# Kernel optimization log

Hardware: AMD Instinct MI355X
Metric: run time of the kernel (lower is better)

## Reference

```python
import jax, jax.numpy as jnp
import numpy as np

N = 100000      # nodes
E = 1600000     # edges (avg degree 16)
F_IN = 512      # input node features
H = 8           # heads in conv1
D = 8           # per-head dim in conv1
C = 7           # classes
NEG_SLOPE = 0.2 # PyG GATConv default leaky_relu slope


def setup_inputs() -> dict:
    key = jax.random.key(0)
    ks = jax.random.split(key, 10)
    s = 0.05
    return {
        "x": jax.random.normal(ks[0], (N, F_IN), jnp.float32),
        "edge_index": jax.random.randint(ks[1], (2, E), 0, N, dtype=jnp.int64),
        "W1": jax.random.normal(ks[2], (F_IN, H * D), jnp.float32) * s,
        "a1_src": jax.random.normal(ks[3], (H, D), jnp.float32) * s,
        "a1_dst": jax.random.normal(ks[4], (H, D), jnp.float32) * s,
        "b1": jnp.zeros((H * D,), jnp.float32),
        "W2": jax.random.normal(ks[5], (H * D, C), jnp.float32) * s,
        "a2_src": jax.random.normal(ks[6], (1, C), jnp.float32) * s,
        "a2_dst": jax.random.normal(ks[7], (1, C), jnp.float32) * s,
        "b2": jnp.zeros((C,), jnp.float32),
    }


def _gat_conv(x, src, dst, W, a_src, a_dst, b, heads, dim, concat, n):
    # linear transform -> [N, H, D]
    h = (x @ W).reshape(n, heads, dim)
    # per-node attention halves: [N, H]
    al_src = jnp.einsum('nhd,hd->nh', h, a_src)
    al_dst = jnp.einsum('nhd,hd->nh', h, a_dst)
    # per-edge logits, leaky relu: [E', H]
    e = jax.nn.leaky_relu(al_src[src] + al_dst[dst], NEG_SLOPE)
    # segment softmax over incoming edges of each dst node
    m = jax.lax.stop_gradient(jax.ops.segment_max(e, dst, num_segments=n))
    p = jnp.exp(e - m[dst])
    z = jax.ops.segment_sum(p, dst, num_segments=n)
    alpha = p / z[dst]                                   # [E', H]
    # weighted scatter-add of source messages -> [N, H, D]
    out = jax.ops.segment_sum(h[src] * alpha[..., None], dst, num_segments=n)
    out = out.reshape(n, heads * dim) if concat else out.mean(axis=1)
    return out + b


def reference(x, edge_index, W1, a1_src, a1_dst, b1, W2, a2_src, a2_dst, b2):
    n = x.shape[0]
    # PyG GATConv default: add self loops
    loops = jnp.arange(n, dtype=edge_index.dtype)
    src = jnp.concatenate([edge_index[0], loops])
    dst = jnp.concatenate([edge_index[1], loops])
    h = _gat_conv(x, src, dst, W1, a1_src, a1_dst, b1, H, D, True, n)
    h = jax.nn.elu(h)
    out = _gat_conv(h, src, dst, W2, a2_src, a2_dst, b2, 1, C, False, n)
    return jax.nn.log_softmax(out, axis=1)
```

## Files before the change

kernel.cpp:

```cpp
#include <hip/hip_runtime.h>
#include <math.h>

#define N_NODES 100000
#define N_EDGES 1600000
#define F_IN 512
#define HD 64
#define CC 7
#define NKT (F_IN / 32)
#define BS 64
#define NBK ((N_NODES + BS - 1) / BS)
#define ECAP 2048
#define SCHUNK 4096
#define SBLK ((N_EDGES + SCHUNK - 1) / SCHUNK)

typedef __attribute__((ext_vector_type(8))) short short8;
typedef __attribute__((ext_vector_type(4))) float f32x4;

__device__ inline unsigned short f2bf(float f) {
    union { float f; unsigned u; } v; v.f = f;
    unsigned u = v.u;
    return (unsigned short)((u + 0x7fffu + ((u >> 16) & 1u)) >> 16);
}
__device__ inline float bf2f(unsigned short b) {
    union { unsigned u; float f; } v; v.u = ((unsigned)b) << 16;
    return v.f;
}

__global__ void zerob_kernel(int* __restrict__ bcur) {
    int i = blockIdx.x * 1024 + threadIdx.x;
    if (i < NBK) bcur[i] = 0;
}

__global__ void w1prep_kernel(const float* __restrict__ W1,
                              unsigned short* __restrict__ wf) {
    int t = blockIdx.x * 256 + threadIdx.x;
    if (t >= NKT * 4 * 64) return;
    int lane = t & 63;
    int ct = (t >> 6) & 3;
    int kt = t >> 8;
    int k0 = kt * 32 + (lane >> 4) * 8;
    int col = ct * 16 + (lane & 15);
    unsigned short* dst = wf + (size_t)t * 8;
    #pragma unroll
    for (int j = 0; j < 8; ++j) dst[j] = f2bf(W1[(k0 + j) * HD + col]);
}

__global__ __launch_bounds__(256) void gemm1att_kernel(const float* __restrict__ x,
                                                       const unsigned short* __restrict__ wf,
                                                       const float* __restrict__ a1s,
                                                       const float* __restrict__ a1d,
                                                       unsigned short* __restrict__ h1b,
                                                       float* __restrict__ als,
                                                       float* __restrict__ ald) {
    __shared__ float ls[64][65];
    const int wave = threadIdx.x >> 6;
    const int lane = threadIdx.x & 63;
    int arow = blockIdx.x * 64 + wave * 16 + (lane & 15);
    if (arow >= N_NODES) arow = N_NODES - 1;
    const float* xp = x + (size_t)arow * F_IN + (lane >> 4) * 8;
    const short8* wp = (const short8*)wf;

    f32x4 acc[4] = {};
    #pragma unroll 4
    for (int kt = 0; kt < NKT; ++kt) {
        f32x4 a0 = *(const f32x4*)(xp + kt * 32);
        f32x4 a1 = *(const f32x4*)(xp + kt * 32 + 4);
        union { short8 s; unsigned short u[8]; } af;
        af.u[0] = f2bf(a0.x); af.u[1] = f2bf(a0.y);
        af.u[2] = f2bf(a0.z); af.u[3] = f2bf(a0.w);
        af.u[4] = f2bf(a1.x); af.u[5] = f2bf(a1.y);
        af.u[6] = f2bf(a1.z); af.u[7] = f2bf(a1.w);
        #pragma unroll
        for (int ct = 0; ct < 4; ++ct) {
            short8 bf = wp[kt * 256 + ct * 64 + lane];
            acc[ct] = __builtin_amdgcn_mfma_f32_16x16x32_bf16(af.s, bf, acc[ct], 0, 0, 0);
        }
    }
    const int lrow_base = wave * 16 + (lane >> 4) * 4;
    const int ocol = lane & 15;
    #pragma unroll
    for (int ct = 0; ct < 4; ++ct) {
        #pragma unroll
        for (int r = 0; r < 4; ++r) {
            int lrow = lrow_base + r;
            int orow = blockIdx.x * 64 + lrow;
            ls[lrow][ct * 16 + ocol] = acc[ct][r];
            if (orow < N_NODES)
                h1b[(size_t)orow * HD + ct * 16 + ocol] = f2bf(acc[ct][r]);
        }
    }
    __syncthreads();
    #pragma unroll
    for (int task = threadIdx.x; task < 64 * 8; task += 256) {
        int r = task >> 3, h = task & 7;
        int node = blockIdx.x * 64 + r;
        if (node < N_NODES) {
            float s = 0.f, d = 0.f;
            #pragma unroll
            for (int k = 0; k < 8; ++k) {
                float v = ls[r][h * 8 + k];
                s += v * a1s[h * 8 + k];
                d += v * a1d[h * 8 + k];
            }
            als[node * 8 + h] = s;
            ald[node * 8 + h] = d;
        }
    }
}

__global__ __launch_bounds__(256) void binscatter_kernel(const int* __restrict__ ei,
                                                         int* __restrict__ bcur,
                                                         int2* __restrict__ pairs) {
    __shared__ int cnt[NBK];
    __shared__ int bas[NBK];
    const int e0 = blockIdx.x * SCHUNK;
    int e1 = e0 + SCHUNK; if (e1 > N_EDGES) e1 = N_EDGES;
    for (int b = threadIdx.x; b < NBK; b += 256) cnt[b] = 0;
    __syncthreads();
    for (int i = e0 + threadIdx.x; i < e1; i += 256)
        atomicAdd(&cnt[ei[N_EDGES + i] >> 6], 1);
    __syncthreads();
    for (int b = threadIdx.x; b < NBK; b += 256) {
        int c = cnt[b];
        bas[b] = c ? atomicAdd(&bcur[b], c) : 0;
        cnt[b] = 0;
    }
    __syncthreads();
    for (int i = e0 + threadIdx.x; i < e1; i += 256) {
        int s = ei[i];
        int t = ei[N_EDGES + i];
        int b = t >> 6;
        int pos = bas[b] + atomicAdd(&cnt[b], 1);
        if (pos < ECAP) pairs[(size_t)b * ECAP + pos] = make_int2(s, t);
    }
}

__global__ __launch_bounds__(256) void sortcsr_kernel(const int* __restrict__ bcur,
                                                      const int2* __restrict__ pairs,
                                                      int* __restrict__ csr_src,
                                                      int* __restrict__ rowptr,
                                                      int* __restrict__ rowcnt) {
    __shared__ int cnt[BS];
    __shared__ int start[BS];
    __shared__ int srcl[ECAP];
    const int tid = threadIdx.x;
    const int lane = tid & 63;
    const int n0 = blockIdx.x * BS;
    const size_t bbase = (size_t)blockIdx.x * ECAP;
    const int2* bp = pairs + bbase;
    int ne = bcur[blockIdx.x]; if (ne > ECAP) ne = ECAP;
    if (tid < BS) cnt[tid] = 0;
    __syncthreads();
    for (int k = tid; k < ne; k += 256)
        atomicAdd(&cnt[bp[k].y & (BS - 1)], 1);
    __syncthreads();
    if (tid < 64) {
        int a = cnt[lane];
        int xx = a;
        #pragma unroll
        for (int o = 1; o < 64; o <<= 1) { int u = __shfl_up(xx, o, 64); if (lane >= o) xx += u; }
        start[lane] = xx - a;
        cnt[lane] = 0;
    }
    __syncthreads();
    for (int k = tid; k < ne; k += 256) {
        int2 pr = bp[k];
        int ln = pr.y & (BS - 1);
        int pos = start[ln] + atomicAdd(&cnt[ln], 1);
        srcl[pos] = pr.x;
    }
    __syncthreads();
    for (int k = tid; k < ne; k += 256) csr_src[bbase + k] = srcl[k];
    if (tid < BS) {
        int node = n0 + tid;
        if (node < N_NODES) {
            rowptr[node] = (int)bbase + start[tid];
            rowcnt[node] = cnt[tid];
        }
    }
}

__global__ __launch_bounds__(256) void gather1_kernel(
        const int* __restrict__ rowptr, const int* __restrict__ rowcnt,
        const int* __restrict__ csr_src,
        const float* __restrict__ als, const float* __restrict__ ald,
        const unsigned short* __restrict__ h1b, const float* __restrict__ b1,
        const float* __restrict__ W2, const float* __restrict__ a2s,
        const float* __restrict__ a2d,
        unsigned short* __restrict__ g2b, float* __restrict__ al2s,
        float* __restrict__ al2d) {
    int node = (blockIdx.x * 256 + threadIdx.x) >> 6;
    if (node >= N_NODES) return;
    const int lane = threadIdx.x & 63;
    const int h = lane >> 3;
    const int e8 = lane & 7, base8 = lane & 56;
    const int rs = rowptr[node], ncnt = rowcnt[node];
    const float aldt = ald[node * 8 + h];
    float e = als[node * 8 + h] + aldt;
    e = (e >= 0.f) ? e : 0.2f * e;
    float p = __expf(e);
    float acc = p * bf2f(h1b[(size_t)node * HD + lane]);
    float z = p;
    int k = 0;
    for (; k + 8 <= ncnt; k += 8) {
        int s_own = csr_src[rs + k + e8];
        int se[8];
        #pragma unroll
        for (int q = 0; q < 8; ++q) se[q] = __shfl(s_own, base8 | q, 64);
        float ve[8];
        #pragma unroll
        for (int q = 0; q < 8; ++q) ve[q] = bf2f(h1b[(size_t)se[q] * HD + lane]);
        float ee = als[s_own * 8 + h] + aldt;
        ee = (ee >= 0.f) ? ee : 0.2f * ee;
        float pv = __expf(ee);
        #pragma unroll
        for (int q = 0; q < 8; ++q) {
            float pe = __shfl(pv, base8 | q, 64);
            z += pe;
            acc = fmaf(pe, ve[q], acc);
        }
    }
    if (k < ncnt) {
        const int m = ncnt - k;
        int idx = rs + k + ((e8 < m) ? e8 : (m - 1));
        int s_own = csr_src[idx];
        int se[8];
        #pragma unroll
        for (int q = 0; q < 8; ++q) se[q] = __shfl(s_own, base8 | q, 64);
        float ee = als[s_own * 8 + h] + aldt;
        ee = (ee >= 0.f) ? ee : 0.2f * ee;
        float pv = __expf(ee);
        for (int q = 0; q < m; ++q) {
            float pe = __shfl(pv, base8 | q, 64);
            float ve = bf2f(h1b[(size_t)se[q] * HD + lane]);
            z += pe;
            acc = fmaf(pe, ve, acc);
        }
    }
    float v = acc / z + b1[lane];
    v = (v > 0.f) ? v : (__expf(v) - 1.f);
    float w[CC];
    #pragma unroll
    for (int c = 0; c < CC; ++c) w[c] = W2[lane * CC + c];
    float g[CC];
    #pragma unroll
    for (int c = 0; c < CC; ++c) {
        float r = v * w[c];
        #pragma unroll
        for (int d = 1; d < 64; d <<= 1) r += __shfl_xor(r, d, 64);
        g[c] = r;
    }
    float s2 = 0.f, d2 = 0.f;
    #pragma unroll
    for (int c = 0; c < CC; ++c) { s2 += g[c] * a2s[c]; d2 += g[c] * a2d[c]; }
    if (lane < CC) g2b[(size_t)node * 8 + lane] = f2bf(g[lane]);
    if (lane == CC) g2b[(size_t)node * 8 + CC] = 0;
    if (lane == 8) al2s[node] = s2;
    if (lane == 9) al2d[node] = d2;
}

__global__ __launch_bounds__(256) void gather2_kernel(
        const int* __restrict__ rowptr, const int* __restrict__ rowcnt,
        const int* __restrict__ csr_src,
        const float* __restrict__ al2s, const float* __restrict__ al2d,
        const unsigned short* __restrict__ g2b, const float* __restrict__ b2,
        float* __restrict__ out) {
    int gid = blockIdx.x * 256 + threadIdx.x;
    int n = gid >> 3, c = gid & 7;
    if (n >= N_NODES) return;
    const int lane = threadIdx.x & 63;
    const int base8 = lane & 56;
    const int rs = rowptr[n], ncnt = rowcnt[n];
    const float adn = al2d[n];
    float e = al2s[n] + adn;
    e = (e >= 0.f) ? e : 0.2f * e;
    float p = __expf(e);
    float acc = p * bf2f(g2b[(size_t)n * 8 + c]);
    float z = p;
    int k = 0;
    for (; k + 8 <= ncnt; k += 8) {
        int s_own = csr_src[rs + k + c];
        int se[8];
        #pragma unroll
        for (int q = 0; q < 8; ++q) se[q] = __shfl(s_own, base8 | q, 64);
        float ve[8];
        #pragma unroll
        for (int q = 0; q < 8; ++q) ve[q] = bf2f(g2b[(size_t)se[q] * 8 + c]);
        float ee = al2s[s_own] + adn;
        ee = (ee >= 0.f) ? ee : 0.2f * ee;
        float pv = __expf(ee);
        #pragma unroll
        for (int q = 0; q < 8; ++q) {
            float pe = __shfl(pv, base8 | q, 64);
            z += pe;
            acc = fmaf(pe, ve[q], acc);
        }
    }
    if (k < ncnt) {
        const int m = ncnt - k;
        int idx = rs + k + ((c < m) ? c : (m - 1));
        int s_own = csr_src[idx];
        int se[8];
        #pragma unroll
        for (int q = 0; q < 8; ++q) se[q] = __shfl(s_own, base8 | q, 64);
        float ee = al2s[s_own] + adn;
        ee = (ee >= 0.f) ? ee : 0.2f * ee;
        float pv = __expf(ee);
        for (int q = 0; q < m; ++q) {
            float pe = __shfl(pv, base8 | q, 64);
            float ve = bf2f(g2b[(size_t)se[q] * 8 + c]);
            z += pe;
            acc = fmaf(pe, ve, acc);
        }
    }
    float o = (c < CC) ? (acc / z + b2[c]) : -1e30f;
    float m2 = o;
    #pragma unroll
    for (int d = 1; d < 8; d <<= 1) m2 = fmaxf(m2, __shfl_xor(m2, d, 8));
    float ex = (c < CC) ? __expf(o - m2) : 0.f;
    float sum = ex;
    #pragma unroll
    for (int d = 1; d < 8; d <<= 1) sum += __shfl_xor(sum, d, 8);
    float lse = m2 + __logf(sum);
    if (c < CC) out[(size_t)n * CC + c] = o - lse;
}

extern "C" void kernel_launch(void* const* d_in, const int* in_sizes, int n_in,
                              void* d_out, int out_size, void* d_ws, size_t ws_size,
                              hipStream_t stream) {
    const float* x   = (const float*)d_in[0];
    const int*   ei  = (const int*)d_in[1];
    const float* W1  = (const float*)d_in[2];
    const float* a1s = (const float*)d_in[3];
    const float* a1d = (const float*)d_in[4];
    const float* b1  = (const float*)d_in[5];
    const float* W2  = (const float*)d_in[6];
    const float* a2s = (const float*)d_in[7];
    const float* a2d = (const float*)d_in[8];
    const float* b2  = (const float*)d_in[9];
    float* out = (float*)d_out;

    char* base = (char*)d_ws;
    size_t off = 0;
    auto alloc = [&](size_t bytes) { char* p = base + off; off = (off + bytes + 63) & ~(size_t)63; return p; };
    unsigned short* h1b = (unsigned short*)alloc((size_t)N_NODES * HD * 2);
    unsigned short* wf  = (unsigned short*)alloc((size_t)NKT * 4 * 64 * 8 * 2);
    float* als  = (float*)alloc((size_t)N_NODES * 8 * 4);
    float* ald  = (float*)alloc((size_t)N_NODES * 8 * 4);
    unsigned short* g2b = (unsigned short*)alloc((size_t)N_NODES * 8 * 2);
    float* al2s = (float*)alloc((size_t)N_NODES * 4);
    float* al2d = (float*)alloc((size_t)N_NODES * 4);
    int* bcur   = (int*)alloc((size_t)NBK * 4);
    int* rowptr = (int*)alloc((size_t)N_NODES * 4);
    int* rowcnt = (int*)alloc((size_t)N_NODES * 4);
    int* csr_src= (int*)alloc((size_t)NBK * ECAP * 4);
    int2* pairs = (int2*)alloc((size_t)NBK * ECAP * 8);

    zerob_kernel<<<(NBK + 1023) / 1024, 1024, 0, stream>>>(bcur);
    w1prep_kernel<<<(NKT * 4 * 64 + 255) / 256, 256, 0, stream>>>(W1, wf);
    binscatter_kernel<<<SBLK, 256, 0, stream>>>(ei, bcur, pairs);
    sortcsr_kernel<<<NBK, 256, 0, stream>>>(bcur, pairs, csr_src, rowptr, rowcnt);

    gemm1att_kernel<<<(N_NODES + 63) / 64, 256, 0, stream>>>(
        x, wf, a1s, a1d, h1b, als, ald);

    gather1_kernel<<<(N_NODES * 64 + 255) / 256, 256, 0, stream>>>(
        rowptr, rowcnt, csr_src, als, ald, h1b, b1, W2, a2s, a2d, g2b, al2s, al2d);
    gather2_kernel<<<(N_NODES * 8 + 255) / 256, 256, 0, stream>>>(
        rowptr, rowcnt, csr_src, al2s, al2d, g2b, b2, out);
}
```

Baseline: 223.5 us.

## Fuse edge binning with GEMM1 in one launch and pack edge pairs into int

Merges the zero and W1-prep kernels into one prep launch, and runs the edge bin-scatter blocks and GEMM1+attention blocks as separate block ranges of a single fused kernel so the two independent phases overlap on the GPU. The (src,dst) pairs are packed into one 32-bit int (src<<6 | local dst), which halves the pair buffer traffic in both scatter and sort. This cuts launch count and lets memory-bound scatter hide behind the MFMA GEMM, at the cost of shared-memory reuse between roles and the packing relying on src fitting in 26 bits.

```diff
diff --git a/kernel.cpp b/kernel.cpp
--- a/kernel.cpp
+++ b/kernel.cpp
@@ -12,6 +12,8 @@
 #define ECAP 2048
 #define SCHUNK 4096
 #define SBLK ((N_EDGES + SCHUNK - 1) / SCHUNK)
+#define GEMMBLKS ((N_NODES + 63) / 64)
+#define W1WORK (NKT * 4 * 64)
 
 typedef __attribute__((ext_vector_type(8))) short short8;
 typedef __attribute__((ext_vector_type(4))) float f32x4;
@@ -26,15 +28,15 @@
     return v.f;
 }
 
-__global__ void zerob_kernel(int* __restrict__ bcur) {
-    int i = blockIdx.x * 1024 + threadIdx.x;
-    if (i < NBK) bcur[i] = 0;
-}
-
-__global__ void w1prep_kernel(const float* __restrict__ W1,
-                              unsigned short* __restrict__ wf) {
+__global__ __launch_bounds__(256) void prep_kernel(const float* __restrict__ W1,
+                                                   unsigned short* __restrict__ wf,
+                                                   int* __restrict__ bcur) {
+    if (blockIdx.x == 16) {
+        for (int i = threadIdx.x; i < NBK; i += 256) bcur[i] = 0;
+        return;
+    }
     int t = blockIdx.x * 256 + threadIdx.x;
-    if (t >= NKT * 4 * 64) return;
+    if (t >= W1WORK) return;
     int lane = t & 63;
     int ct = (t >> 6) & 3;
     int kt = t >> 8;
@@ -45,17 +47,44 @@
     for (int j = 0; j < 8; ++j) dst[j] = f2bf(W1[(k0 + j) * HD + col]);
 }
 
-__global__ __launch_bounds__(256) void gemm1att_kernel(const float* __restrict__ x,
-                                                       const unsigned short* __restrict__ wf,
-                                                       const float* __restrict__ a1s,
-                                                       const float* __restrict__ a1d,
-                                                       unsigned short* __restrict__ h1b,
-                                                       float* __restrict__ als,
-                                                       float* __restrict__ ald) {
-    __shared__ float ls[64][65];
-    const int wave = threadIdx.x >> 6;
-    const int lane = threadIdx.x & 63;
-    int arow = blockIdx.x * 64 + wave * 16 + (lane & 15);
+__global__ __launch_bounds__(256) void fused_kernel(
+        const int* __restrict__ ei, int* __restrict__ bcur, int* __restrict__ pairs,
+        const float* __restrict__ x, const unsigned short* __restrict__ wf,
+        const float* __restrict__ a1s, const float* __restrict__ a1d,
+        unsigned short* __restrict__ h1b, float* __restrict__ als,
+        float* __restrict__ ald) {
+    __shared__ float ls[64 * 65];
+    const int bid = blockIdx.x;
+    const int tid = threadIdx.x;
+    if (bid < SBLK) {
+        int* cnt = (int*)ls;
+        int* bas = cnt + NBK;
+        const int e0 = bid * SCHUNK;
+        int e1 = e0 + SCHUNK; if (e1 > N_EDGES) e1 = N_EDGES;
+        for (int b = tid; b < NBK; b += 256) cnt[b] = 0;
+        __syncthreads();
+        for (int i = e0 + tid; i < e1; i += 256)
+            atomicAdd(&cnt[ei[N_EDGES + i] >> 6], 1);
+        __syncthreads();
+        for (int b = tid; b < NBK; b += 256) {
+            int c = cnt[b];
+            bas[b] = c ? atomicAdd(&bcur[b], c) : 0;
+            cnt[b] = 0;
+        }
+        __syncthreads();
+        for (int i = e0 + tid; i < e1; i += 256) {
+            int s = ei[i];
+            int t = ei[N_EDGES + i];
+            int b = t >> 6;
+            int pos = bas[b] + atomicAdd(&cnt[b], 1);
+            if (pos < ECAP) pairs[(size_t)b * ECAP + pos] = (s << 6) | (t & (BS - 1));
+        }
+        return;
+    }
+    const int gb = bid - SBLK;
+    const int wave = tid >> 6;
+    const int lane = tid & 63;
+    int arow = gb * 64 + wave * 16 + (lane & 15);
     if (arow >= N_NODES) arow = N_NODES - 1;
     const float* xp = x + (size_t)arow * F_IN + (lane >> 4) * 8;
     const short8* wp = (const short8*)wf;
@@ -83,22 +112,22 @@
         #pragma unroll
         for (int r = 0; r < 4; ++r) {
             int lrow = lrow_base + r;
-            int orow = blockIdx.x * 64 + lrow;
-            ls[lrow][ct * 16 + ocol] = acc[ct][r];
+            int orow = gb * 64 + lrow;
+            ls[lrow * 65 + ct * 16 + ocol] = acc[ct][r];
             if (orow < N_NODES)
                 h1b[(size_t)orow * HD + ct * 16 + ocol] = f2bf(acc[ct][r]);
         }
     }
     __syncthreads();
     #pragma unroll
-    for (int task = threadIdx.x; task < 64 * 8; task += 256) {
+    for (int task = tid; task < 64 * 8; task += 256) {
         int r = task >> 3, h = task & 7;
-        int node = blockIdx.x * 64 + r;
+        int node = gb * 64 + r;
         if (node < N_NODES) {
             float s = 0.f, d = 0.f;
             #pragma unroll
             for (int k = 0; k < 8; ++k) {
-                float v = ls[r][h * 8 + k];
+                float v = ls[r * 65 + h * 8 + k];
                 s += v * a1s[h * 8 + k];
                 d += v * a1d[h * 8 + k];
             }
@@ -108,35 +137,8 @@
     }
 }
 
-__global__ __launch_bounds__(256) void binscatter_kernel(const int* __restrict__ ei,
-                                                         int* __restrict__ bcur,
-                                                         int2* __restrict__ pairs) {
-    __shared__ int cnt[NBK];
-    __shared__ int bas[NBK];
-    const int e0 = blockIdx.x * SCHUNK;
-    int e1 = e0 + SCHUNK; if (e1 > N_EDGES) e1 = N_EDGES;
-    for (int b = threadIdx.x; b < NBK; b += 256) cnt[b] = 0;
-    __syncthreads();
-    for (int i = e0 + threadIdx.x; i < e1; i += 256)
-        atomicAdd(&cnt[ei[N_EDGES + i] >> 6], 1);
-    __syncthreads();
-    for (int b = threadIdx.x; b < NBK; b += 256) {
-        int c = cnt[b];
-        bas[b] = c ? atomicAdd(&bcur[b], c) : 0;
-        cnt[b] = 0;
-    }
-    __syncthreads();
-    for (int i = e0 + threadIdx.x; i < e1; i += 256) {
-        int s = ei[i];
-        int t = ei[N_EDGES + i];
-        int b = t >> 6;
-        int pos = bas[b] + atomicAdd(&cnt[b], 1);
-        if (pos < ECAP) pairs[(size_t)b * ECAP + pos] = make_int2(s, t);
-    }
-}
-
 __global__ __launch_bounds__(256) void sortcsr_kernel(const int* __restrict__ bcur,
-                                                      const int2* __restrict__ pairs,
+                                                      const int* __restrict__ pairs,
                                                       int* __restrict__ csr_src,
                                                       int* __restrict__ rowptr,
                                                       int* __restrict__ rowcnt) {
@@ -147,12 +149,12 @@
     const int lane = tid & 63;
     const int n0 = blockIdx.x * BS;
     const size_t bbase = (size_t)blockIdx.x * ECAP;
-    const int2* bp = pairs + bbase;
+    const int* bp = pairs + bbase;
     int ne = bcur[blockIdx.x]; if (ne > ECAP) ne = ECAP;
     if (tid < BS) cnt[tid] = 0;
     __syncthreads();
     for (int k = tid; k < ne; k += 256)
-        atomicAdd(&cnt[bp[k].y & (BS - 1)], 1);
+        atomicAdd(&cnt[bp[k] & (BS - 1)], 1);
     __syncthreads();
     if (tid < 64) {
         int a = cnt[lane];
@@ -164,10 +166,10 @@
     }
     __syncthreads();
     for (int k = tid; k < ne; k += 256) {
-        int2 pr = bp[k];
-        int ln = pr.y & (BS - 1);
+        int v = bp[k];
+        int ln = v & (BS - 1);
         int pos = start[ln] + atomicAdd(&cnt[ln], 1);
-        srcl[pos] = pr.x;
+        srcl[pos] = v >> 6;
     }
     __syncthreads();
     for (int k = tid; k < ne; k += 256) csr_src[bbase + k] = srcl[k];
@@ -344,7 +346,7 @@
     size_t off = 0;
     auto alloc = [&](size_t bytes) { char* p = base + off; off = (off + bytes + 63) & ~(size_t)63; return p; };
     unsigned short* h1b = (unsigned short*)alloc((size_t)N_NODES * HD * 2);
-    unsigned short* wf  = (unsigned short*)alloc((size_t)NKT * 4 * 64 * 8 * 2);
+    unsigned short* wf  = (unsigned short*)alloc((size_t)W1WORK * 8 * 2);
     float* als  = (float*)alloc((size_t)N_NODES * 8 * 4);
     float* ald  = (float*)alloc((size_t)N_NODES * 8 * 4);
     unsigned short* g2b = (unsigned short*)alloc((size_t)N_NODES * 8 * 2);
@@ -354,16 +356,12 @@
     int* rowptr = (int*)alloc((size_t)N_NODES * 4);
     int* rowcnt = (int*)alloc((size_t)N_NODES * 4);
     int* csr_src= (int*)alloc((size_t)NBK * ECAP * 4);
-    int2* pairs = (int2*)alloc((size_t)NBK * ECAP * 8);
-
-    zerob_kernel<<<(NBK + 1023) / 1024, 1024, 0, stream>>>(bcur);
-    w1prep_kernel<<<(NKT * 4 * 64 + 255) / 256, 256, 0, stream>>>(W1, wf);
-    binscatter_kernel<<<SBLK, 256, 0, stream>>>(ei, bcur, pairs);
+    int* pairs  = (int*)alloc((size_t)NBK * ECAP * 4);
+
+    prep_kernel<<<17, 256, 0, stream>>>(W1, wf, bcur);
+    fused_kernel<<<SBLK + GEMMBLKS, 256, 0, stream>>>(
+        ei, bcur, pairs, x, wf, a1s, a1d, h1b, als, ald);
     sortcsr_kernel<<<NBK, 256, 0, stream>>>(bcur, pairs, csr_src, rowptr, rowcnt);
-
-    gemm1att_kernel<<<(N_NODES + 63) / 64, 256, 0, stream>>>(
-        x, wf, a1s, a1d, h1b, als, ald);
-
     gather1_kernel<<<(N_NODES * 64 + 255) / 256, 256, 0, stream>>>(
         rowptr, rowcnt, csr_src, als, ald, h1b, b1, W2, a2s, a2d, g2b, al2s, al2d);
     gather2_kernel<<<(N_NODES * 8 + 255) / 256, 256, 0, stream>>>(
```

Result: faster. 200.5 us (-10.3%).
